# Kernel optimization log

Hardware: AMD Instinct MI355X
Metric: run time of the kernel (lower is better)

Reference implementation:

```python
import jax, jax.numpy as jnp
import numpy as np

KS = 3   # window kernel size
NH = 4   # num heads

def unfold3d(x, ks):
    # x: (B,C,D,H,W) -> (B,C,D*H*W, ks**3); matches torch unfold(2).unfold(3).unfold(4) ordering
    B, C, D, H, W = x.shape
    p = ks // 2
    xp = jnp.pad(x, ((0,0),(0,0),(p,p),(p,p),(p,p)))
    wins = [xp[:, :, i:i+D, j:j+H, k:k+W]
            for i in range(ks) for j in range(ks) for k in range(ks)]
    u = jnp.stack(wins, axis=-1)  # (B,C,D,H,W,ks^3)
    return u.reshape(B, C, D*H*W, ks**3)

def make_mask(D, H, W, ks):
    ones = jnp.ones((1, 1, D, H, W), jnp.float32)
    return unfold3d(ones, ks)[0, 0] == 0  # (N, ks^3), True = out-of-bounds (masked)

def l2norm(x, eps=1e-12):
    n = jnp.sqrt(jnp.sum(x * x, axis=-1, keepdims=True))
    return x / jnp.maximum(n, eps)

def layernorm(x, g, b, eps=1e-5):
    m = x.mean(-1, keepdims=True)
    v = x.var(-1, keepdims=True)
    return (x - m) / jnp.sqrt(v + eps) * g + b

def conv3d(x, w, b, pad):
    y = jax.lax.conv_general_dilated(x, w, (1,1,1), [(pad,pad)]*3,
        dimension_numbers=('NCDHW', 'OIDHW', 'NCDHW'))
    return y + b.reshape(1, -1, 1, 1, 1)

def bnorm(x, g, b, eps=1e-5):
    # BatchNorm3d, training-mode batch statistics (biased variance)
    m = x.mean(axis=(0,2,3,4), keepdims=True)
    v = ((x - m) ** 2).mean(axis=(0,2,3,4), keepdims=True)
    return (x - m) / jnp.sqrt(v + eps) * g.reshape(1,-1,1,1,1) + b.reshape(1,-1,1,1,1)

def lrelu(x):
    return jnp.where(x > 0, x, 0.01 * x)

def resblock(x, w1, b1, g1, be1, w2, b2, g2, be2):
    # monai UnetResBlock, in==out, stride 1 -> identity residual
    y = lrelu(bnorm(conv3d(x, w1, b1, 1), g1, be1))
    y = bnorm(conv3d(y, w2, b2, 1), g2, be2)
    return lrelu(y + x)

def epa(x, D, H, W, mask, qkvv_w, temp, temp2, rpb, qemb, op1_w, op1_b, op2_w, op2_b):
    B, N, C = x.shape
    hd = C // NH
    qkvv = (x @ qkvv_w.T).reshape(B, N, 4, NH, hd).transpose(2, 0, 3, 1, 4)  # (4,B,NH,N,hd)
    q, k, v_ca, v_sa = qkvv[0], qkvv[1], qkvv[2], qkvv[3]
    # ---- spatial (local window) attention ----
    qns = (l2norm(q) + qemb) * jax.nn.softplus(temp2)  # (B,NH,N,hd)
    k_flat = k.transpose(0, 1, 3, 2).reshape(B, C, N)
    v_flat = v_sa.transpose(0, 1, 3, 2).reshape(B, C, N)
    k_loc = unfold3d(k_flat.reshape(B, C, D, H, W), KS).reshape(B, NH, hd, N, KS**3).transpose(0, 1, 3, 2, 4)
    v_loc = unfold3d(v_flat.reshape(B, C, D, H, W), KS).reshape(B, NH, hd, N, KS**3).transpose(0, 1, 3, 2, 4)
    attn_sa = jnp.einsum('bhnd,bhndk->bhnk', qns, k_loc) + rpb[None, :, None, :]
    attn_sa = jnp.where(mask[None, None], -jnp.inf, attn_sa)
    attn_sa = jax.nn.softmax(attn_sa, axis=-1)
    # NOTE: original torch code reshapes (B,NH,N,hd) directly to (B,N,C); replicate exactly
    x_sa = jnp.einsum('bhnk,bhndk->bhnd', attn_sa, v_loc).reshape(B, N, C)
    # ---- channel (cosine) cross-attention ----
    qt = l2norm(q.transpose(0, 1, 3, 2))  # (B,NH,hd,N), normalized over N
    kt = l2norm(k.transpose(0, 1, 3, 2))
    attn_ca = jax.nn.softmax(jnp.einsum('bhdn,bhen->bhde', qt, kt) * temp, axis=-1)
    x_ca = jnp.einsum('bhde,bhen->bhdn', attn_ca, v_ca.transpose(0, 1, 3, 2)).transpose(0, 3, 1, 2).reshape(B, N, C)
    return jnp.concatenate([x_sa @ op1_w.T + op1_b, x_ca @ op2_w.T + op2_b], axis=-1)


def setup_inputs() -> dict:
    key = jax.random.key(0)
    B, C, H, W, D = 1, 64, 32, 32, 32
    hd = C // NH
    ks = iter(jax.random.split(key, 40))
    def nrm(shape, s=0.02):
        return jax.random.normal(next(ks), shape, jnp.float32) * s
    inp = {
        'x': jax.random.normal(next(ks), (B, C, H, W, D), jnp.float32),
        'ln_g': jnp.ones((C,), jnp.float32), 'ln_b': jnp.zeros((C,), jnp.float32),
        'gamma': 1e-6 * jnp.ones((C,), jnp.float32),
        'qkvv_w': nrm((4 * C, C)),
        'temp': jnp.ones((NH, 1, 1), jnp.float32), 'temp2': jnp.ones((NH, 1, 1), jnp.float32),
        'rpb': nrm((NH, KS**3), 4e-4),
        'qemb': nrm((NH, 1, hd)),
        'op1_w': nrm((C // 2, C)), 'op1_b': jnp.zeros((C // 2,), jnp.float32),
        'op2_w': nrm((C // 2, C)), 'op2_b': jnp.zeros((C // 2,), jnp.float32),
    }
    for name in ('c51', 'c52'):
        inp[name + '_w1'] = nrm((C, C, 3, 3, 3)); inp[name + '_b1'] = jnp.zeros((C,), jnp.float32)
        inp[name + '_g1'] = jnp.ones((C,), jnp.float32); inp[name + '_be1'] = jnp.zeros((C,), jnp.float32)
        inp[name + '_w2'] = nrm((C, C, 3, 3, 3)); inp[name + '_b2'] = jnp.zeros((C,), jnp.float32)
        inp[name + '_g2'] = jnp.ones((C,), jnp.float32); inp[name + '_be2'] = jnp.zeros((C,), jnp.float32)
    inp['c8_w'] = nrm((C, C, 1, 1, 1)); inp['c8_b'] = jnp.zeros((C,), jnp.float32)
    return inp


def reference(x, ln_g, ln_b, gamma, qkvv_w, temp, temp2, rpb, qemb,
              op1_w, op1_b, op2_w, op2_b,
              c51_w1, c51_b1, c51_g1, c51_be1, c51_w2, c51_b2, c51_g2, c51_be2,
              c52_w1, c52_b1, c52_g1, c52_be1, c52_w2, c52_b2, c52_g2, c52_be2,
              c8_w, c8_b):
    B, C, H, W, D = x.shape
    N = H * W * D
    xs = x.reshape(B, C, N).transpose(0, 2, 1)  # (B,N,C)
    mask = make_mask(D, H, W, KS)
    attn = xs + gamma * epa(layernorm(xs, ln_g, ln_b), D, H, W, mask,
                            qkvv_w, temp, temp2, rpb, qemb, op1_w, op1_b, op2_w, op2_b)
    skip = attn.reshape(B, H, W, D, C).transpose(0, 4, 1, 2, 3)  # (B,C,H,W,D)
    y = resblock(skip, c51_w1, c51_b1, c51_g1, c51_be1, c51_w2, c51_b2, c51_g2, c51_be2)
    y = resblock(y, c52_w1, c52_b1, c52_g1, c52_be1, c52_w2, c52_b2, c52_g2, c52_be2)
    return skip + conv3d(y, c8_w, c8_b, 0)
```

## Files before the change

kernel.cpp:

```cpp
#include <hip/hip_runtime.h>
#include <hip/hip_bf16.h>

typedef __hip_bfloat16 bf16;
typedef __attribute__((ext_vector_type(8))) short s8v;
typedef __attribute__((ext_vector_type(4))) float f4v;

#define NTOT 32768
#define PADV 39304
#define HSZ ((size_t)NTOT*16)

__device__ __forceinline__ float bflo(unsigned int u){ union{unsigned int i;float f;}v; v.i=u<<16; return v.f; }
__device__ __forceinline__ float bfhi(unsigned int u){ union{unsigned int i;float f;}v; v.i=u&0xffff0000u; return v.f; }
__device__ __forceinline__ unsigned short f2bu(float f){ bf16 h = __float2bfloat16(f); unsigned short s; __builtin_memcpy(&s,&h,2); return s; }
__device__ __forceinline__ unsigned int pk2(float a, float b){ return (unsigned int)f2bu(a) | ((unsigned int)f2bu(b)<<16); }

__device__ __forceinline__ void load8(const bf16* p, float* o){
  uint4 u = *(const uint4*)p;
  o[0]=bflo(u.x); o[1]=bfhi(u.x); o[2]=bflo(u.y); o[3]=bfhi(u.y);
  o[4]=bflo(u.z); o[5]=bfhi(u.z); o[6]=bflo(u.w); o[7]=bfhi(u.w);
}
__device__ __forceinline__ void load16(const bf16* p, float* o){
  const uint4* q = (const uint4*)p;
  uint4 u0 = q[0], u1 = q[1];
  o[0]=bflo(u0.x); o[1]=bfhi(u0.x); o[2]=bflo(u0.y); o[3]=bfhi(u0.y);
  o[4]=bflo(u0.z); o[5]=bfhi(u0.z); o[6]=bflo(u0.w); o[7]=bfhi(u0.w);
  o[8]=bflo(u1.x); o[9]=bfhi(u1.x); o[10]=bflo(u1.y); o[11]=bfhi(u1.y);
  o[12]=bflo(u1.z); o[13]=bfhi(u1.z); o[14]=bflo(u1.w); o[15]=bfhi(u1.w);
}
__device__ __forceinline__ void store16(bf16* p, const float* v){
  uint4 u0, u1;
  u0.x=pk2(v[0],v[1]); u0.y=pk2(v[2],v[3]); u0.z=pk2(v[4],v[5]); u0.w=pk2(v[6],v[7]);
  u1.x=pk2(v[8],v[9]); u1.y=pk2(v[10],v[11]); u1.z=pk2(v[12],v[13]); u1.w=pk2(v[14],v[15]);
  uint4* q=(uint4*)p; q[0]=u0; q[1]=u1;
}

__global__ __launch_bounds__(256) void k_qkvv(const float* __restrict__ x,
    const float* __restrict__ lng, const float* __restrict__ lnb,
    const float* __restrict__ w,
    bf16* __restrict__ Qh, bf16* __restrict__ Kh, bf16* __restrict__ Vsh, bf16* __restrict__ Vch)
{
  __shared__ unsigned char sm[64000];
  float* xt = (float*)sm;
  float* mean_s = (float*)(sm + 16896);
  float* rstd_s = (float*)(sm + 16896 + 256);
  float* g_s    = (float*)(sm + 16896 + 512);
  float* b_s    = (float*)(sm + 16896 + 768);
  unsigned char* A2 = sm + 17920;
  unsigned char* Wb = sm + 27136;
  unsigned char* Cout = sm;

  int t = threadIdx.x;
  int n0 = blockIdx.x * 64;
  #pragma unroll
  for (int i=0;i<4;i++){
    int idx = t + i*256; int c = idx>>4, g = idx&15;
    *(float4*)&xt[c*66 + g*4] = *(const float4*)(x + (size_t)c*NTOT + n0 + g*4);
  }
  #pragma unroll
  for (int i=0;i<8;i++){
    int idx = t + i*256; int j = idx>>3, g = idx&7;
    float4 wa = *(const float4*)(w + (size_t)j*64 + g*8);
    float4 wb = *(const float4*)(w + (size_t)j*64 + g*8 + 4);
    uint4 u; u.x=pk2(wa.x,wa.y); u.y=pk2(wa.z,wa.w); u.z=pk2(wb.x,wb.y); u.w=pk2(wb.z,wb.w);
    *(uint4*)(Wb + j*144 + g*16) = u;
  }
  if (t<64){ g_s[t]=lng[t]; b_s[t]=lnb[t]; }
  __syncthreads();
  if (t<64){
    float s=0.f, ss=0.f;
    for (int c=0;c<64;c++){ float v=xt[c*66+t]; s+=v; ss+=v*v; }
    float m = s*(1.f/64.f);
    float var = ss*(1.f/64.f) - m*m;
    mean_s[t]=m; rstd_s[t]=rsqrtf(var+1e-5f);
  }
  __syncthreads();
  {
    int p = t>>2, c0 = (t&3)*16;
    float m = mean_s[p], rs = rstd_s[p];
    unsigned short tmp[16];
    #pragma unroll
    for (int i=0;i<16;i++){
      int c = c0+i;
      tmp[i] = f2bu((xt[c*66+p]-m)*rs*g_s[c] + b_s[c]);
    }
    *(uint4*)(A2 + p*144 + c0*2)      = *(uint4*)&tmp[0];
    *(uint4*)(A2 + p*144 + c0*2 + 16) = *(uint4*)&tmp[8];
  }
  __syncthreads();
  int wv = t>>6, lane = t&63, r = lane&15, q = lane>>4;
  f4v acc[4][4];
  #pragma unroll
  for (int mt=0;mt<4;mt++)
    #pragma unroll
    for (int nt=0;nt<4;nt++){ acc[mt][nt][0]=0.f; acc[mt][nt][1]=0.f; acc[mt][nt][2]=0.f; acc[mt][nt][3]=0.f; }
  #pragma unroll
  for (int ks=0; ks<2; ++ks){
    s8v af[4], bfr[4];
    #pragma unroll
    for (int mt=0;mt<4;mt++) af[mt] = *(const s8v*)(A2 + (mt*16+r)*144 + ks*64 + q*16);
    #pragma unroll
    for (int nt=0;nt<4;nt++) bfr[nt] = *(const s8v*)(Wb + ((wv*4+nt)*16+r)*144 + ks*64 + q*16);
    #pragma unroll
    for (int mt=0;mt<4;mt++)
      #pragma unroll
      for (int nt=0;nt<4;nt++)
        acc[mt][nt] = __builtin_amdgcn_mfma_f32_16x16x32_bf16(af[mt], bfr[nt], acc[mt][nt], 0, 0, 0);
  }
  __syncthreads();
  #pragma unroll
  for (int mt=0;mt<4;mt++)
    #pragma unroll
    for (int nt=0;nt<4;nt++){
      int j = (wv*4+nt)*16 + r;
      #pragma unroll
      for (int reg=0;reg<4;reg++){
        int p = mt*16 + q*4 + reg;
        *(unsigned short*)(Cout + p*528 + j*2) = f2bu(acc[mt][nt][reg]);
      }
    }
  __syncthreads();
  bf16* bases[4] = {Qh, Kh, Vch, Vsh};
  #pragma unroll
  for (int k=0;k<4;k++){
    int chunk = t + k*256;
    int combo = chunk >> 6, pos = chunk & 63;
    int tensor = combo >> 2, h = combo & 3;
    uint4 v = *(const uint4*)(Cout + pos*528 + (tensor*64 + h*16)*2);
    *(uint4*)((unsigned char*)bases[tensor] + ((size_t)h*HSZ + (size_t)(n0+pos)*16)*2) = v;
  }
}

__global__ __launch_bounds__(256) void k_chanpart(const bf16* __restrict__ Qh, const bf16* __restrict__ Kh,
    float* __restrict__ G, float* __restrict__ NQ, float* __restrict__ NK)
{
  int h = blockIdx.y;
  int t = threadIdx.x; int d = t>>4, e = t&15;
  __shared__ float qs[128][16];
  __shared__ float ks[128][16];
  float acc=0.f, accq=0.f, acck=0.f;
  for (int stage=0; stage<2; ++stage){
    int n0 = blockIdx.x*256 + stage*128;
    __syncthreads();
    {
      int row = t & 127, which = t >> 7;
      const bf16* p = (which ? Kh : Qh) + ((size_t)h*NTOT + n0 + row)*16;
      float tmp[16]; load16(p, tmp);
      float* dst = which ? &ks[row][0] : &qs[row][0];
      #pragma unroll
      for (int i=0;i<16;i++) dst[i]=tmp[i];
    }
    __syncthreads();
    for (int i=0;i<128;i++){
      float qv = qs[i][d], kv = ks[i][e];
      acc += qv*kv;
      if (e==0) accq += qv*qv;
      if (e==1){ float kd = ks[i][d]; acck += kd*kd; }
    }
  }
  atomicAdd(&G[(h*16+d)*16+e], acc);
  if (e==0) atomicAdd(&NQ[h*16+d], accq);
  if (e==1) atomicAdd(&NK[h*16+d], acck);
}

__global__ __launch_bounds__(256) void k_spatial(const bf16* __restrict__ Qh, const bf16* __restrict__ Kh,
    const bf16* __restrict__ Vsh, const bf16* __restrict__ Vch,
    const float* __restrict__ G, const float* __restrict__ NQ, const float* __restrict__ NK,
    const float* __restrict__ temp, const float* __restrict__ temp2,
    const float* __restrict__ rpb, const float* __restrict__ qemb,
    bf16* __restrict__ xsa, bf16* __restrict__ xca)
{
  __shared__ float aca_s[1024];
  __shared__ float rpb_s[108];
  __shared__ float qemb_s[64];
  int t = threadIdx.x;
  if (t < 64){
    int hh = t>>4;
    float tp = temp[hh];
    float nq = fmaxf(sqrtf(NQ[t]), 1e-12f);
    float sv[16]; float mx=-3.0e38f;
    #pragma unroll
    for (int e=0;e<16;e++){
      float nk = fmaxf(sqrtf(NK[hh*16+e]), 1e-12f);
      sv[e] = G[t*16+e] / (nq*nk) * tp;
      mx = fmaxf(mx, sv[e]);
    }
    float sum=0.f;
    #pragma unroll
    for (int e=0;e<16;e++){ sv[e]=expf(sv[e]-mx); sum+=sv[e]; }
    float inv = 1.f/sum;
    #pragma unroll
    for (int e=0;e<16;e++) aca_s[t*16+e] = sv[e]*inv;
  }
  if (t<108) rpb_s[t]=rpb[t];
  if (t<64) qemb_s[t]=qemb[t];
  __syncthreads();
  int lane = t & 63, h = t >> 6;
  int n = blockIdx.x*64 + lane;
  int a = n>>10, b=(n>>5)&31, c=n&31;
  const bf16* Kb = Kh + (size_t)h*HSZ;
  const bf16* Vb = Vsh + (size_t)h*HSZ;
  float q[16]; load16(Qh + (size_t)h*HSZ + (size_t)n*16, q);
  float s2=0.f;
  #pragma unroll
  for (int d=0;d<16;d++) s2 += q[d]*q[d];
  float inv = 1.f/fmaxf(sqrtf(s2), 1e-12f);
  float st2 = log1pf(expf(temp2[h]));
  #pragma unroll
  for (int d=0;d<16;d++) q[d] = (q[d]*inv + qemb_s[h*16+d])*st2;
  float sc[27]; float mx = -3.0e38f;
  #pragma unroll
  for (int kk=0;kk<27;kk++){
    int da=kk/9-1, db=(kk/3)%3-1, dc=kk%3-1;
    int aa=a+da, bb=b+db, cc=c+dc;
    float s = -3.0e38f;
    if ((unsigned)aa<32u && (unsigned)bb<32u && (unsigned)cc<32u){
      int nn = n + da*1024 + db*32 + dc;
      float kv[16]; load16(Kb + (size_t)nn*16, kv);
      s = rpb_s[h*27+kk];
      #pragma unroll
      for (int d=0;d<16;d++) s += q[d]*kv[d];
    }
    sc[kk]=s; mx = fmaxf(mx, s);
  }
  float sum=0.f;
  #pragma unroll
  for (int kk=0;kk<27;kk++){ float e = expf(sc[kk]-mx); sc[kk]=e; sum+=e; }
  float invs = 1.f/sum;
  float o[16];
  #pragma unroll
  for (int d=0;d<16;d++) o[d]=0.f;
  #pragma unroll
  for (int kk=0;kk<27;kk++){
    int da=kk/9-1, db=(kk/3)%3-1, dc=kk%3-1;
    int aa=a+da, bb=b+db, cc=c+dc;
    if ((unsigned)aa<32u && (unsigned)bb<32u && (unsigned)cc<32u){
      int nn = n + da*1024 + db*32 + dc;
      float vv[16]; load16(Vb + (size_t)nn*16, vv);
      float p = sc[kk];
      #pragma unroll
      for (int d=0;d<16;d++) o[d] += p*vv[d];
    }
  }
  #pragma unroll
  for (int d=0;d<16;d++) o[d]*=invs;
  store16(xsa + ((size_t)h*NTOT + n)*16, o);
  float vca[16]; load16(Vch + (size_t)h*HSZ + (size_t)n*16, vca);
  float oc[16];
  #pragma unroll
  for (int d=0;d<16;d++){
    float s=0.f;
    #pragma unroll
    for (int e=0;e<16;e++) s += aca_s[(h*16+d)*16+e]*vca[e];
    oc[d]=s;
  }
  store16(xca + (size_t)n*64 + h*16, oc);
}

__global__ __launch_bounds__(256) void k_epilogue(const float* __restrict__ x,
    const bf16* __restrict__ xsa, const bf16* __restrict__ xca,
    const float* __restrict__ op1w, const float* __restrict__ op1b,
    const float* __restrict__ op2w, const float* __restrict__ op2b,
    const float* __restrict__ gamma, float* __restrict__ skip)
{
  __shared__ float xs_s[64][68];
  __shared__ float xc_s[64][68];
  int t = threadIdx.x;
  int n0 = blockIdx.x * 64;
  #pragma unroll
  for (int it=0; it<2; ++it){
    int idx = t + it*256;
    int p = idx >> 3, cg = idx & 7;
    float a8[8], c8[8];
    load8(xsa + (size_t)(n0+p)*64 + cg*8, a8);
    load8(xca + (size_t)(n0+p)*64 + cg*8, c8);
    #pragma unroll
    for (int i=0;i<8;i++){ xs_s[p][cg*8+i]=a8[i]; xc_s[p][cg*8+i]=c8[i]; }
  }
  int co = t & 63, pg = t >> 6;
  const float* wrow = (co < 32) ? (op1w + (size_t)co*64) : (op2w + (size_t)(co-32)*64);
  float wreg[64];
  #pragma unroll
  for (int i=0;i<16;i++) *(float4*)&wreg[i*4] = *(const float4*)(wrow + i*4);
  float bv = (co<32) ? op1b[co] : op2b[co-32];
  float gv = gamma[co];
  __syncthreads();
  const float* xt = (co<32) ? &xs_s[0][0] : &xc_s[0][0];
  float out16[16];
  #pragma unroll
  for (int i=0;i<16;i++){
    int p = pg*16 + i;
    const float* xr = xt + p*68;
    float s = bv;
    #pragma unroll
    for (int k4=0;k4<16;k4++){
      float4 xv = *(const float4*)(xr + k4*4);
      s += wreg[k4*4]*xv.x + wreg[k4*4+1]*xv.y + wreg[k4*4+2]*xv.z + wreg[k4*4+3]*xv.w;
    }
    out16[i] = s;
  }
  size_t base = (size_t)co*NTOT + n0 + pg*16;
  #pragma unroll
  for (int i4=0;i4<4;i4++){
    float4 xv = *(const float4*)(x + base + i4*4);
    float4 ov;
    ov.x = xv.x + gv*out16[i4*4];
    ov.y = xv.y + gv*out16[i4*4+1];
    ov.z = xv.z + gv*out16[i4*4+2];
    ov.w = xv.w + gv*out16[i4*4+3];
    *(float4*)(skip + base + i4*4) = ov;
  }
}

__global__ void k_wprep(const float* __restrict__ wA, const float* __restrict__ wB_,
    const float* __restrict__ wC, const float* __restrict__ wD,
    const float* __restrict__ w8, bf16* __restrict__ WB, float* __restrict__ w8t)
{
  int idx = blockIdx.x*256 + threadIdx.x;
  if (idx < 458752){
    int j = idx & 7;
    int rr = (idx>>3) & 15;
    int q = (idx>>7) & 3;
    int nt = (idx>>9) & 3;
    int rest = idx >> 11;
    int tp = rest % 14;
    int rest2 = rest / 14;
    int cc = rest2 & 3;
    int conv = rest2 >> 2;
    int co = nt*16 + rr;
    int tap = 2*tp + (q>>1);
    int ci = cc*16 + (q&1)*8 + j;
    const float* src = conv==0?wA:conv==1?wB_:conv==2?wC:wD;
    float v = (tap < 27) ? src[((size_t)co*64 + ci)*27 + tap] : 0.f;
    WB[idx] = __float2bfloat16(v);
  }
  if (idx < 4096){ int ci = idx>>6, co = idx&63; w8t[ci*64+co] = w8[(size_t)co*64+ci]; }
}

__global__ __launch_bounds__(256) void k_padt0(const float* __restrict__ src, bf16* __restrict__ xpt)
{
  __shared__ bf16 tile[32][68];
  int t = threadIdx.x;
  int n0 = blockIdx.x * 32;
  int nl = t & 31, cig = t >> 5;
  int n = n0 + nl;
  #pragma unroll
  for (int i=0;i<8;i++){
    int ci = cig*8 + i;
    tile[nl][ci] = __float2bfloat16(src[(size_t)ci*NTOT + n]);
  }
  __syncthreads();
  int a = n0 >> 10, b = (n0 >> 5) & 31;
  size_t rowbase = ((size_t)((a+1)*34 + (b+1))*34 + 1)*64;
  #pragma unroll
  for (int k2=0;k2<2;k2++){
    int j = t + k2*256;
    int nn = j >> 4, grp = j & 15;
    uint2 val = *(const uint2*)&tile[nn][grp*4];
    *(uint2*)((unsigned char*)xpt + (rowbase + (size_t)nn*64 + grp*4)*2) = val;
  }
}

__global__ __launch_bounds__(256) void k_padtbn(const bf16* __restrict__ src,
    const float* __restrict__ stats, const float* __restrict__ g, const float* __restrict__ be,
    const float* __restrict__ skipin, bf16* __restrict__ xpt)
{
  __shared__ bf16 tile[32][68];
  int t = threadIdx.x;
  int n0 = blockIdx.x * 32;
  int nl = t & 31, cig = t >> 5;
  int n = n0 + nl;
  #pragma unroll
  for (int i=0;i<8;i++){
    int ci = cig*8 + i;
    float S = stats[ci*2], SS = stats[ci*2+1];
    float m = S*(1.f/NTOT);
    float rs = rsqrtf(SS*(1.f/NTOT) - m*m + 1e-5f);
    float v = __bfloat162float(src[(size_t)ci*NTOT + n]);
    v = (v-m)*rs*g[ci] + be[ci];
    if (skipin) v += skipin[(size_t)ci*NTOT + n];
    v = v>0.f ? v : 0.01f*v;
    tile[nl][ci] = __float2bfloat16(v);
  }
  __syncthreads();
  int a = n0 >> 10, b = (n0 >> 5) & 31;
  size_t rowbase = ((size_t)((a+1)*34 + (b+1))*34 + 1)*64;
  #pragma unroll
  for (int k2=0;k2<2;k2++){
    int j = t + k2*256;
    int nn = j >> 4, grp = j & 15;
    uint2 val = *(const uint2*)&tile[nn][grp*4];
    *(uint2*)((unsigned char*)xpt + (rowbase + (size_t)nn*64 + grp*4)*2) = val;
  }
}

__global__ __launch_bounds__(256, 2) void k_conv3m(const bf16* __restrict__ xpt,
    const bf16* __restrict__ WB, const float* __restrict__ bias,
    bf16* __restrict__ Yb, float* __restrict__ BNpart)
{
  __shared__ float smf[17408];
  unsigned char* smb = (unsigned char*)smf;
  int t = threadIdx.x;
  int w = t >> 6, lane = t & 63;
  int r = lane & 15, q = lane >> 4;
  int qe = q & 1, qh = q >> 1;
  int xcd = blockIdx.x & 7, loc = blockIdx.x >> 3;
  int a = xcd*4 + (loc>>4), b0 = (loc&15)*2;

  {
    uint4 tmp[13];
    #pragma unroll
    for (int k=0;k<13;k++){
      int idx = t + k*256;
      if (idx < 3264){
        int pos = idx >> 3, h = idx & 7;
        int par = pos/136, rem = pos - par*136;
        int pbr = rem/34, pc = rem - pbr*34;
        size_t gb = (((size_t)(a+par)*34 + (b0+pbr))*34 + pc)*128 + h*16;
        tmp[k] = *(const uint4*)((const unsigned char*)xpt + gb);
      }
    }
    #pragma unroll
    for (int k=0;k<13;k++){
      int idx = t + k*256;
      if (idx < 3264){
        int pos = idx >> 3, h = idx & 7;
        *(uint4*)(smb + pos*144 + h*16) = tmp[k];
      }
    }
  }

  int toff[14];
  #pragma unroll
  for (int tp=0;tp<14;++tp){
    int tap = 2*tp + qh;
    int da = tap/9, rem = tap - da*9, db = rem/3, dc = rem - db*3;
    toff[tp] = (tap<27) ? (((da*4+db)*34 + dc)*144) : 0;
  }
  int F[4];
  #pragma unroll
  for (int mt=0;mt<4;mt++) F[mt] = (((mt>>1)*34 + (mt&1)*16 + r)*144) + w*32 + qe*16;
  const unsigned char* wbp = (const unsigned char*)WB + (size_t)w*57344 + lane*16;

  f4v acc[4][4];
  #pragma unroll
  for (int mt=0;mt<4;mt++)
    #pragma unroll
    for (int nt=0;nt<4;nt++){ acc[mt][nt][0]=0.f; acc[mt][nt][1]=0.f; acc[mt][nt][2]=0.f; acc[mt][nt][3]=0.f; }

  __syncthreads();

  s8v aC[4], bC[4], bN[4];
  #pragma unroll
  for (int mt=0;mt<4;mt++) aC[mt] = *(const s8v*)(smb + F[mt] + toff[0]);
  #pragma unroll
  for (int nt=0;nt<4;nt++){ bC[nt] = *(const s8v*)(wbp + nt*1024); bN[nt] = *(const s8v*)(wbp + 4096 + nt*1024); }

  #pragma unroll
  for (int tp=0; tp<14; ++tp){
    s8v aN[4], bN2[4];
    if (tp < 12){
      #pragma unroll
      for (int nt=0;nt<4;nt++) bN2[nt] = *(const s8v*)(wbp + (tp+2)*4096 + nt*1024);
    }
    if (tp < 13){
      #pragma unroll
      for (int mt=0;mt<4;mt++) aN[mt] = *(const s8v*)(smb + F[mt] + toff[tp+1]);
    }
    #pragma unroll
    for (int mt=0;mt<4;mt++)
      #pragma unroll
      for (int nt=0;nt<4;nt++)
        acc[mt][nt] = __builtin_amdgcn_mfma_f32_16x16x32_bf16(aC[mt], bC[nt], acc[mt][nt], 0, 0, 0);
    #pragma unroll
    for (int nt=0;nt<4;nt++) bC[nt] = bN[nt];
    if (tp < 12){
      #pragma unroll
      for (int nt=0;nt<4;nt++) bN[nt] = bN2[nt];
    }
    if (tp < 13){
      #pragma unroll
      for (int mt=0;mt<4;mt++) aC[mt] = aN[mt];
    }
  }

  __syncthreads();
  #pragma unroll
  for (int mt=0;mt<4;mt++)
    #pragma unroll
    for (int nt=0;nt<4;nt++)
      *(float4*)&smf[w*4352 + (nt*16+r)*68 + mt*16 + q*4] = *(float4*)&acc[mt][nt];
  __syncthreads();

  {
    int co = t >> 2, pg = t & 3;
    float bv = bias[co];
    float vals[16];
    #pragma unroll
    for (int i4=0;i4<4;i4++){
      int p = pg*16 + i4*4;
      float4 s0 = *(const float4*)&smf[0*4352 + co*68 + p];
      float4 s1 = *(const float4*)&smf[1*4352 + co*68 + p];
      float4 s2 = *(const float4*)&smf[2*4352 + co*68 + p];
      float4 s3 = *(const float4*)&smf[3*4352 + co*68 + p];
      vals[i4*4+0] = s0.x+s1.x+s2.x+s3.x+bv;
      vals[i4*4+1] = s0.y+s1.y+s2.y+s3.y+bv;
      vals[i4*4+2] = s0.z+s1.z+s2.z+s3.z+bv;
      vals[i4*4+3] = s0.w+s1.w+s2.w+s3.w+bv;
    }
    float s=0.f, ss=0.f;
    #pragma unroll
    for (int i=0;i<16;i++){ s+=vals[i]; ss+=vals[i]*vals[i]; }
    s += __shfl_xor(s,1); ss += __shfl_xor(ss,1);
    s += __shfl_xor(s,2); ss += __shfl_xor(ss,2);
    if (pg==0){
      BNpart[(size_t)blockIdx.x*128 + co*2]     = s;
      BNpart[(size_t)blockIdx.x*128 + co*2 + 1] = ss;
    }
    uint4 u0, u1;
    u0.x=pk2(vals[0],vals[1]); u0.y=pk2(vals[2],vals[3]); u0.z=pk2(vals[4],vals[5]); u0.w=pk2(vals[6],vals[7]);
    u1.x=pk2(vals[8],vals[9]); u1.y=pk2(vals[10],vals[11]); u1.z=pk2(vals[12],vals[13]); u1.w=pk2(vals[14],vals[15]);
    size_t nb = (size_t)co*NTOT + (size_t)a*1024 + b0*32 + pg*16;
    uint4* dst = (uint4*)((unsigned char*)Yb + nb*2);
    dst[0] = u0; dst[1] = u1;
  }
}

__global__ __launch_bounds__(1024) void k_bnred(const float* __restrict__ BNpart, float* __restrict__ BNout)
{
  __shared__ float red[8][128];
  int t = threadIdx.x;
  int col = t & 127, grp = t >> 7;
  float acc = 0.f;
  #pragma unroll 8
  for (int r = grp*64; r < grp*64 + 64; ++r) acc += BNpart[r*128 + col];
  red[grp][col] = acc;
  __syncthreads();
  if (grp == 0){
    float s = 0.f;
    #pragma unroll
    for (int g=0; g<8; g++) s += red[g][col];
    BNout[col] = s;
  }
}

__global__ __launch_bounds__(256) void k_conv1f(const bf16* __restrict__ Y2b,
    const float* __restrict__ BNst, const float* __restrict__ g, const float* __restrict__ be,
    const bf16* __restrict__ xptR, const float* __restrict__ w8t, const float* __restrict__ b8,
    const float* __restrict__ skip, float* __restrict__ out)
{
  __shared__ unsigned short xptt[64][72];
  __shared__ float R2[64][68];
  __shared__ float wt[4096];
  __shared__ float bs[64];
  int t = threadIdx.x;
  int n0 = blockIdx.x * 64;
  int a = n0 >> 10, b0 = (n0 >> 5) & 31;
  {
    int p = t >> 2, seg = t & 3;
    int pb = b0 + (p >> 5) + 1, pc = (p & 31) + 1;
    size_t rowb = (((size_t)(a+1)*34 + pb)*34 + pc)*128;
    uint4 v0 = *(const uint4*)((const unsigned char*)xptR + rowb + seg*32);
    uint4 v1 = *(const uint4*)((const unsigned char*)xptR + rowb + seg*32 + 16);
    *(uint4*)((unsigned char*)&xptt[p][seg*16]) = v0;
    *(uint4*)((unsigned char*)&xptt[p][seg*16 + 8]) = v1;
  }
  #pragma unroll
  for (int k=0;k<4;k++){
    int idx = t + k*256;
    *(float4*)&wt[idx*4] = *(const float4*)(w8t + idx*4);
  }
  if (t < 64) bs[t] = b8[t];
  __syncthreads();
  {
    int ci = t >> 2, pg = t & 3;
    float S = BNst[ci*2], SS = BNst[ci*2+1];
    float m = S*(1.f/NTOT);
    float rs = rsqrtf(SS*(1.f/NTOT) - m*m + 1e-5f);
    float gv = g[ci], bev = be[ci];
    float y16[16];
    load16(Y2b + (size_t)ci*NTOT + n0 + pg*16, y16);
    #pragma unroll
    for (int i=0;i<16;i++){
      int nl = pg*16 + i;
      unsigned short us = xptt[nl][ci];
      union{unsigned int ui; float f;} cv; cv.ui = ((unsigned int)us)<<16;
      float v = (y16[i]-m)*rs*gv + bev + cv.f;
      R2[ci][nl] = v>0.f ? v : 0.01f*v;
    }
  }
  __syncthreads();
  int lane = t & 63, cg = t >> 6;
  float acc[16];
  #pragma unroll
  for (int j=0;j<16;j++) acc[j]=0.f;
  for (int ci=0; ci<64; ci++){
    float rv = R2[ci][lane];
    const float* wr = &wt[ci*64 + cg*16];
    float4 wa = *(const float4*)(wr);
    float4 wb = *(const float4*)(wr+4);
    float4 wc = *(const float4*)(wr+8);
    float4 wd = *(const float4*)(wr+12);
    acc[0]+=rv*wa.x; acc[1]+=rv*wa.y; acc[2]+=rv*wa.z; acc[3]+=rv*wa.w;
    acc[4]+=rv*wb.x; acc[5]+=rv*wb.y; acc[6]+=rv*wb.z; acc[7]+=rv*wb.w;
    acc[8]+=rv*wc.x; acc[9]+=rv*wc.y; acc[10]+=rv*wc.z; acc[11]+=rv*wc.w;
    acc[12]+=rv*wd.x; acc[13]+=rv*wd.y; acc[14]+=rv*wd.z; acc[15]+=rv*wd.w;
  }
  #pragma unroll
  for (int j=0;j<16;j++){
    int co = cg*16+j;
    out[(size_t)co*NTOT + n0 + lane] = acc[j] + bs[co] + skip[(size_t)co*NTOT + n0 + lane];
  }
}

extern "C" void kernel_launch(void* const* d_in, const int* in_sizes, int n_in,
                              void* d_out, int out_size, void* d_ws, size_t ws_size,
                              hipStream_t stream) {
  (void)in_sizes; (void)n_in; (void)out_size; (void)ws_size;
  const float* x      = (const float*)d_in[0];
  const float* ln_g   = (const float*)d_in[1];
  const float* ln_b   = (const float*)d_in[2];
  const float* gamma  = (const float*)d_in[3];
  const float* qkvv_w = (const float*)d_in[4];
  const float* temp   = (const float*)d_in[5];
  const float* temp2  = (const float*)d_in[6];
  const float* rpb    = (const float*)d_in[7];
  const float* qemb   = (const float*)d_in[8];
  const float* op1w   = (const float*)d_in[9];
  const float* op1b   = (const float*)d_in[10];
  const float* op2w   = (const float*)d_in[11];
  const float* op2b   = (const float*)d_in[12];
  const float* c51_w1 = (const float*)d_in[13];
  const float* c51_b1 = (const float*)d_in[14];
  const float* c51_g1 = (const float*)d_in[15];
  const float* c51_be1= (const float*)d_in[16];
  const float* c51_w2 = (const float*)d_in[17];
  const float* c51_b2 = (const float*)d_in[18];
  const float* c51_g2 = (const float*)d_in[19];
  const float* c51_be2= (const float*)d_in[20];
  const float* c52_w1 = (const float*)d_in[21];
  const float* c52_b1 = (const float*)d_in[22];
  const float* c52_g1 = (const float*)d_in[23];
  const float* c52_be1= (const float*)d_in[24];
  const float* c52_w2 = (const float*)d_in[25];
  const float* c52_b2 = (const float*)d_in[26];
  const float* c52_g2 = (const float*)d_in[27];
  const float* c52_be2= (const float*)d_in[28];
  const float* c8_w   = (const float*)d_in[29];
  const float* c8_b   = (const float*)d_in[30];

  unsigned char* ws = (unsigned char*)d_ws;
  const size_t MB = 1u<<20;
  bf16*  Qh   = (bf16*)(ws + 0);
  bf16*  Kh   = (bf16*)(ws + 4*MB);
  bf16*  Vsh  = (bf16*)(ws + 8*MB);
  bf16*  Vch  = (bf16*)(ws + 12*MB);
  bf16*  xpt  = (bf16*)(ws + 0);
  bf16*  xpt2 = (bf16*)(ws + 5030912);
  bf16*  xsa  = (bf16*)(ws + 16*MB);
  bf16*  xca  = (bf16*)(ws + 20*MB);
  float* skip = (float*)(ws + 24*MB);
  float* stat = (float*)(ws + 32*MB);
  float* G    = stat + 0;
  float* NQ   = stat + 1024;
  float* NK   = stat + 1088;
  float* BN1  = stat + 1152;
  float* BN2  = stat + 1312;
  float* BN3  = stat + 1472;
  float* BN4  = stat + 1632;
  bf16*  WB   = (bf16*)(ws + 32*MB + 65536);
  float* w8t  = (float*)(ws + 32*MB + 65536 + 1835008);
  float* BNpart = (float*)(ws + 34*MB);
  bf16*  Yb   = (bf16*)(ws + 35*MB);
  bf16*  Y2b  = (bf16*)(ws + 39*MB);

  hipMemsetAsync(stat, 0, 1152*sizeof(float), stream);
  k_wprep<<<1792,256,0,stream>>>(c51_w1, c51_w2, c52_w1, c52_w2, c8_w, WB, w8t);
  k_qkvv<<<512,256,0,stream>>>(x, ln_g, ln_b, qkvv_w, Qh, Kh, Vsh, Vch);
  k_chanpart<<<dim3(128,4),256,0,stream>>>(Qh, Kh, G, NQ, NK);
  k_spatial<<<512,256,0,stream>>>(Qh, Kh, Vsh, Vch, G, NQ, NK, temp, temp2, rpb, qemb, xsa, xca);
  k_epilogue<<<512,256,0,stream>>>(x, xsa, xca, op1w, op1b, op2w, op2b, gamma, skip);
  hipMemsetAsync(ws, 0, 2*5030912, stream);
  k_padt0 <<<1024,256,0,stream>>>(skip, xpt);
  k_conv3m<<<512,256,0,stream>>>(xpt, WB + 0*114688, c51_b1, Yb, BNpart);
  k_bnred<<<1,1024,0,stream>>>(BNpart, BN1);
  k_padtbn<<<1024,256,0,stream>>>(Yb, BN1, c51_g1, c51_be1, nullptr, xpt);
  k_conv3m<<<512,256,0,stream>>>(xpt, WB + 1*114688, c51_b2, Y2b, BNpart);
  k_bnred<<<1,1024,0,stream>>>(BNpart, BN2);
  k_padtbn<<<1024,256,0,stream>>>(Y2b, BN2, c51_g2, c51_be2, skip, xpt);
  k_conv3m<<<512,256,0,stream>>>(xpt, WB + 2*114688, c52_b1, Yb, BNpart);
  k_bnred<<<1,1024,0,stream>>>(BNpart, BN3);
  k_padtbn<<<1024,256,0,stream>>>(Yb, BN3, c52_g1, c52_be1, nullptr, xpt2);
  k_conv3m<<<512,256,0,stream>>>(xpt2, WB + 3*114688, c52_b2, Y2b, BNpart);
  k_bnred<<<1,1024,0,stream>>>(BNpart, BN4);
  k_conv1f<<<512,256,0,stream>>>(Y2b, BN4, c52_g2, c52_be2, xpt, w8t, c8_b, skip, (float*)d_out);
}
```

Baseline: 317.0 us.

## Fuse BN/LReLU/pad prologue into conv kernels and switch to channels-last layouts

Removes the separate padding/BN-apply kernels and the padded-buffer memset. Each 3x3x3 conv now loads its input halo directly from an unpadded channels-last tensor, applying the previous BatchNorm, residual add and LeakyReLU on the fly with zero-fill at the borders. The epilogue and conv outputs are transposed through shared memory so they are written channels-last. The final 1x1 conv recomputes the first resblock's output from Y2 and the BN2 stats, so no padded copy is needed. This cuts several launches and a full-tensor write/read per stage, at the cost of extra shared-memory transposes and redundant BN math inside the conv halo loads.

```diff
diff --git a/kernel.cpp b/kernel.cpp
--- a/kernel.cpp
+++ b/kernel.cpp
@@ -6,7 +6,6 @@
 typedef __attribute__((ext_vector_type(4))) float f4v;
 
 #define NTOT 32768
-#define PADV 39304
 #define HSZ ((size_t)NTOT*16)
 
 __device__ __forceinline__ float bflo(unsigned int u){ union{unsigned int i;float f;}v; v.i=u<<16; return v.f; }
@@ -260,10 +259,11 @@
     const bf16* __restrict__ xsa, const bf16* __restrict__ xca,
     const float* __restrict__ op1w, const float* __restrict__ op1b,
     const float* __restrict__ op2w, const float* __restrict__ op2b,
-    const float* __restrict__ gamma, float* __restrict__ skip)
+    const float* __restrict__ gamma, float* __restrict__ skipf)
 {
   __shared__ float xs_s[64][68];
   __shared__ float xc_s[64][68];
+  __shared__ float trans[64][68];
   int t = threadIdx.x;
   int n0 = blockIdx.x * 64;
   #pragma unroll
@@ -302,12 +302,20 @@
   #pragma unroll
   for (int i4=0;i4<4;i4++){
     float4 xv = *(const float4*)(x + base + i4*4);
-    float4 ov;
-    ov.x = xv.x + gv*out16[i4*4];
-    ov.y = xv.y + gv*out16[i4*4+1];
-    ov.z = xv.z + gv*out16[i4*4+2];
-    ov.w = xv.w + gv*out16[i4*4+3];
-    *(float4*)(skip + base + i4*4) = ov;
+    out16[i4*4]   = xv.x + gv*out16[i4*4];
+    out16[i4*4+1] = xv.y + gv*out16[i4*4+1];
+    out16[i4*4+2] = xv.z + gv*out16[i4*4+2];
+    out16[i4*4+3] = xv.w + gv*out16[i4*4+3];
+  }
+  #pragma unroll
+  for (int i=0;i<16;i++) trans[pg*16+i][co] = out16[i];
+  __syncthreads();
+  {
+    int pos = t >> 2, grp = t & 3;
+    float* dst = skipf + (size_t)(n0+pos)*64 + grp*16;
+    #pragma unroll
+    for (int i4=0;i4<4;i4++)
+      *(float4*)(dst + i4*4) = *(const float4*)&trans[pos][grp*16 + i4*4];
   }
 }
 
@@ -336,66 +344,12 @@
   if (idx < 4096){ int ci = idx>>6, co = idx&63; w8t[ci*64+co] = w8[(size_t)co*64+ci]; }
 }
 
-__global__ __launch_bounds__(256) void k_padt0(const float* __restrict__ src, bf16* __restrict__ xpt)
-{
-  __shared__ bf16 tile[32][68];
-  int t = threadIdx.x;
-  int n0 = blockIdx.x * 32;
-  int nl = t & 31, cig = t >> 5;
-  int n = n0 + nl;
-  #pragma unroll
-  for (int i=0;i<8;i++){
-    int ci = cig*8 + i;
-    tile[nl][ci] = __float2bfloat16(src[(size_t)ci*NTOT + n]);
-  }
-  __syncthreads();
-  int a = n0 >> 10, b = (n0 >> 5) & 31;
-  size_t rowbase = ((size_t)((a+1)*34 + (b+1))*34 + 1)*64;
-  #pragma unroll
-  for (int k2=0;k2<2;k2++){
-    int j = t + k2*256;
-    int nn = j >> 4, grp = j & 15;
-    uint2 val = *(const uint2*)&tile[nn][grp*4];
-    *(uint2*)((unsigned char*)xpt + (rowbase + (size_t)nn*64 + grp*4)*2) = val;
-  }
-}
-
-__global__ __launch_bounds__(256) void k_padtbn(const bf16* __restrict__ src,
+template<int MODE>
+__global__ __launch_bounds__(256, 2) void k_conv3x(const void* __restrict__ src,
     const float* __restrict__ stats, const float* __restrict__ g, const float* __restrict__ be,
-    const float* __restrict__ skipin, bf16* __restrict__ xpt)
-{
-  __shared__ bf16 tile[32][68];
-  int t = threadIdx.x;
-  int n0 = blockIdx.x * 32;
-  int nl = t & 31, cig = t >> 5;
-  int n = n0 + nl;
-  #pragma unroll
-  for (int i=0;i<8;i++){
-    int ci = cig*8 + i;
-    float S = stats[ci*2], SS = stats[ci*2+1];
-    float m = S*(1.f/NTOT);
-    float rs = rsqrtf(SS*(1.f/NTOT) - m*m + 1e-5f);
-    float v = __bfloat162float(src[(size_t)ci*NTOT + n]);
-    v = (v-m)*rs*g[ci] + be[ci];
-    if (skipin) v += skipin[(size_t)ci*NTOT + n];
-    v = v>0.f ? v : 0.01f*v;
-    tile[nl][ci] = __float2bfloat16(v);
-  }
-  __syncthreads();
-  int a = n0 >> 10, b = (n0 >> 5) & 31;
-  size_t rowbase = ((size_t)((a+1)*34 + (b+1))*34 + 1)*64;
-  #pragma unroll
-  for (int k2=0;k2<2;k2++){
-    int j = t + k2*256;
-    int nn = j >> 4, grp = j & 15;
-    uint2 val = *(const uint2*)&tile[nn][grp*4];
-    *(uint2*)((unsigned char*)xpt + (rowbase + (size_t)nn*64 + grp*4)*2) = val;
-  }
-}
-
-__global__ __launch_bounds__(256, 2) void k_conv3m(const bf16* __restrict__ xpt,
+    const float* __restrict__ resid,
     const bf16* __restrict__ WB, const float* __restrict__ bias,
-    bf16* __restrict__ Yb, float* __restrict__ BNpart)
+    bf16* __restrict__ Yout, float* __restrict__ BNpart)
 {
   __shared__ float smf[17408];
   unsigned char* smb = (unsigned char*)smf;
@@ -403,28 +357,113 @@
   int w = t >> 6, lane = t & 63;
   int r = lane & 15, q = lane >> 4;
   int qe = q & 1, qh = q >> 1;
-  int xcd = blockIdx.x & 7, loc = blockIdx.x >> 3;
-  int a = xcd*4 + (loc>>4), b0 = (loc&15)*2;
-
-  {
-    uint4 tmp[13];
-    #pragma unroll
-    for (int k=0;k<13;k++){
-      int idx = t + k*256;
-      if (idx < 3264){
-        int pos = idx >> 3, h = idx & 7;
-        int par = pos/136, rem = pos - par*136;
-        int pbr = rem/34, pc = rem - pbr*34;
-        size_t gb = (((size_t)(a+par)*34 + (b0+pbr))*34 + pc)*128 + h*16;
-        tmp[k] = *(const uint4*)((const unsigned char*)xpt + gb);
+  int a = blockIdx.x >> 4, b0 = (blockIdx.x & 15) * 2;
+  int hh = t & 7;
+
+  float m8[8], rs8[8], be8[8];
+  if (MODE != 0){
+    #pragma unroll
+    for (int i=0;i<8;i++){
+      int ci = hh*8 + i;
+      float S = stats[ci*2], SS = stats[ci*2+1];
+      float m = S*(1.f/NTOT);
+      m8[i] = m;
+      rs8[i] = rsqrtf(SS*(1.f/NTOT) - m*m + 1e-5f) * g[ci];
+      be8[i] = be[ci];
+    }
+  }
+
+  if (MODE == 0){
+    #pragma unroll
+    for (int c0=0;c0<2;++c0){
+      int kb = c0*7, kn = (c0==0)?7:6;
+      float4 f0[7], f1[7]; int fl[7];
+      #pragma unroll
+      for (int k=0;k<7;k++){
+        fl[k]=0;
+        if (k<kn){
+          int idx = t + (kb+k)*256;
+          if (idx < 3264){
+            int pos = idx>>3;
+            int par=pos/136, rem=pos-par*136, pbr=rem/34, pc=rem-pbr*34;
+            int pa=a+par, pb=b0+pbr;
+            fl[k]=1;
+            if (pa>=1&&pa<=32&&pb>=1&&pb<=32&&pc>=1&&pc<=32){
+              int nsrc=(pa-1)*1024+(pb-1)*32+(pc-1);
+              const float* p = (const float*)src + (size_t)nsrc*64 + hh*8;
+              f0[k]=*(const float4*)p; f1[k]=*(const float4*)(p+4);
+              fl[k]=2;
+            }
+          }
+        }
       }
-    }
-    #pragma unroll
-    for (int k=0;k<13;k++){
-      int idx = t + k*256;
-      if (idx < 3264){
-        int pos = idx >> 3, h = idx & 7;
-        *(uint4*)(smb + pos*144 + h*16) = tmp[k];
+      #pragma unroll
+      for (int k=0;k<7;k++){
+        if (k<kn && fl[k]){
+          int pos = (t + (kb+k)*256)>>3;
+          uint4 o={0,0,0,0};
+          if (fl[k]==2){
+            o.x=pk2(f0[k].x,f0[k].y); o.y=pk2(f0[k].z,f0[k].w);
+            o.z=pk2(f1[k].x,f1[k].y); o.w=pk2(f1[k].z,f1[k].w);
+          }
+          *(uint4*)(smb + pos*144 + hh*16) = o;
+        }
+      }
+    }
+  } else {
+    const int CS = (MODE==2)?5:13;
+    const int NC = (MODE==2)?3:1;
+    #pragma unroll
+    for (int c0=0;c0<NC;++c0){
+      int kb = c0*CS;
+      int kn = (MODE==2) ? ((c0==2)?3:5) : 13;
+      uint4 u[CS]; float4 r0[CS], r1[CS]; int fl[CS];
+      #pragma unroll
+      for (int k=0;k<CS;k++){
+        fl[k]=0;
+        if (k<kn){
+          int idx = t + (kb+k)*256;
+          if (idx < 3264){
+            int pos = idx>>3;
+            int par=pos/136, rem=pos-par*136, pbr=rem/34, pc=rem-pbr*34;
+            int pa=a+par, pb=b0+pbr;
+            fl[k]=1;
+            if (pa>=1&&pa<=32&&pb>=1&&pb<=32&&pc>=1&&pc<=32){
+              int nsrc=(pa-1)*1024+(pb-1)*32+(pc-1);
+              u[k] = *(const uint4*)((const unsigned char*)src + ((size_t)nsrc*64 + hh*8)*2);
+              if (MODE==2){
+                const float* rp = resid + (size_t)nsrc*64 + hh*8;
+                r0[k]=*(const float4*)rp; r1[k]=*(const float4*)(rp+4);
+              }
+              fl[k]=2;
+            }
+          }
+        }
+      }
+      #pragma unroll
+      for (int k=0;k<CS;k++){
+        if (k<kn && fl[k]){
+          int pos = (t + (kb+k)*256)>>3;
+          uint4 o={0,0,0,0};
+          if (fl[k]==2){
+            float v[8];
+            v[0]=bflo(u[k].x); v[1]=bfhi(u[k].x); v[2]=bflo(u[k].y); v[3]=bfhi(u[k].y);
+            v[4]=bflo(u[k].z); v[5]=bfhi(u[k].z); v[6]=bflo(u[k].w); v[7]=bfhi(u[k].w);
+            float rv[8];
+            if (MODE==2){
+              rv[0]=r0[k].x; rv[1]=r0[k].y; rv[2]=r0[k].z; rv[3]=r0[k].w;
+              rv[4]=r1[k].x; rv[5]=r1[k].y; rv[6]=r1[k].z; rv[7]=r1[k].w;
+            }
+            #pragma unroll
+            for (int i=0;i<8;i++){
+              float y = (v[i]-m8[i])*rs8[i] + be8[i];
+              if (MODE==2) y += rv[i];
+              v[i] = y>0.f ? y : 0.01f*y;
+            }
+            o.x=pk2(v[0],v[1]); o.y=pk2(v[2],v[3]); o.z=pk2(v[4],v[5]); o.w=pk2(v[6],v[7]);
+          }
+          *(uint4*)(smb + pos*144 + hh*16) = o;
+        }
       }
     }
   }
@@ -491,10 +530,10 @@
       *(float4*)&smf[w*4352 + (nt*16+r)*68 + mt*16 + q*4] = *(float4*)&acc[mt][nt];
   __syncthreads();
 
+  float vals[16];
   {
     int co = t >> 2, pg = t & 3;
     float bv = bias[co];
-    float vals[16];
     #pragma unroll
     for (int i4=0;i4<4;i4++){
       int p = pg*16 + i4*4;
@@ -516,11 +555,24 @@
       BNpart[(size_t)blockIdx.x*128 + co*2]     = s;
       BNpart[(size_t)blockIdx.x*128 + co*2 + 1] = ss;
     }
+  }
+  __syncthreads();
+  {
+    int co = t >> 2, pg = t & 3;
+    #pragma unroll
+    for (int i=0;i<16;i++) smf[(pg*16+i)*68 + co] = vals[i];
+  }
+  __syncthreads();
+  {
+    int pos = t >> 2, grp = t & 3;
+    float v16[16];
+    #pragma unroll
+    for (int i4=0;i4<4;i4++) *(float4*)&v16[i4*4] = *(const float4*)&smf[pos*68 + grp*16 + i4*4];
     uint4 u0, u1;
-    u0.x=pk2(vals[0],vals[1]); u0.y=pk2(vals[2],vals[3]); u0.z=pk2(vals[4],vals[5]); u0.w=pk2(vals[6],vals[7]);
-    u1.x=pk2(vals[8],vals[9]); u1.y=pk2(vals[10],vals[11]); u1.z=pk2(vals[12],vals[13]); u1.w=pk2(vals[14],vals[15]);
-    size_t nb = (size_t)co*NTOT + (size_t)a*1024 + b0*32 + pg*16;
-    uint4* dst = (uint4*)((unsigned char*)Yb + nb*2);
+    u0.x=pk2(v16[0],v16[1]); u0.y=pk2(v16[2],v16[3]); u0.z=pk2(v16[4],v16[5]); u0.w=pk2(v16[6],v16[7]);
+    u1.x=pk2(v16[8],v16[9]); u1.y=pk2(v16[10],v16[11]); u1.z=pk2(v16[12],v16[13]); u1.w=pk2(v16[14],v16[15]);
+    int nb = a*1024 + (b0 + (pos>>5))*32 + (pos&31);
+    uint4* dst = (uint4*)((unsigned char*)Yout + ((size_t)nb*64 + grp*16)*2);
     dst[0] = u0; dst[1] = u1;
   }
 }
@@ -543,49 +595,48 @@
   }
 }
 
-__global__ __launch_bounds__(256) void k_conv1f(const bf16* __restrict__ Y2b,
-    const float* __restrict__ BNst, const float* __restrict__ g, const float* __restrict__ be,
-    const bf16* __restrict__ xptR, const float* __restrict__ w8t, const float* __restrict__ b8,
-    const float* __restrict__ skip, float* __restrict__ out)
+__global__ __launch_bounds__(256) void k_conv1f(const bf16* __restrict__ Y4,
+    const float* __restrict__ BN4, const float* __restrict__ g4, const float* __restrict__ be4,
+    const bf16* __restrict__ Y2, const float* __restrict__ BN2,
+    const float* __restrict__ g2, const float* __restrict__ be2,
+    const float* __restrict__ skipf, const float* __restrict__ w8t, const float* __restrict__ b8,
+    float* __restrict__ out)
 {
-  __shared__ unsigned short xptt[64][72];
   __shared__ float R2[64][68];
+  __shared__ float skT[64][68];
   __shared__ float wt[4096];
   __shared__ float bs[64];
   int t = threadIdx.x;
   int n0 = blockIdx.x * 64;
-  int a = n0 >> 10, b0 = (n0 >> 5) & 31;
-  {
-    int p = t >> 2, seg = t & 3;
-    int pb = b0 + (p >> 5) + 1, pc = (p & 31) + 1;
-    size_t rowb = (((size_t)(a+1)*34 + pb)*34 + pc)*128;
-    uint4 v0 = *(const uint4*)((const unsigned char*)xptR + rowb + seg*32);
-    uint4 v1 = *(const uint4*)((const unsigned char*)xptR + rowb + seg*32 + 16);
-    *(uint4*)((unsigned char*)&xptt[p][seg*16]) = v0;
-    *(uint4*)((unsigned char*)&xptt[p][seg*16 + 8]) = v1;
-  }
   #pragma unroll
   for (int k=0;k<4;k++){
     int idx = t + k*256;
     *(float4*)&wt[idx*4] = *(const float4*)(w8t + idx*4);
   }
   if (t < 64) bs[t] = b8[t];
-  __syncthreads();
   {
-    int ci = t >> 2, pg = t & 3;
-    float S = BNst[ci*2], SS = BNst[ci*2+1];
-    float m = S*(1.f/NTOT);
-    float rs = rsqrtf(SS*(1.f/NTOT) - m*m + 1e-5f);
-    float gv = g[ci], bev = be[ci];
-    float y16[16];
-    load16(Y2b + (size_t)ci*NTOT + n0 + pg*16, y16);
+    int pos = t >> 2, grp = t & 3;
+    int n = n0 + pos;
+    float y2[16], y4[16], sk[16];
+    load16(Y2 + (size_t)n*64 + grp*16, y2);
+    load16(Y4 + (size_t)n*64 + grp*16, y4);
+    #pragma unroll
+    for (int i4=0;i4<4;i4++) *(float4*)&sk[i4*4] = *(const float4*)(skipf + (size_t)n*64 + grp*16 + i4*4);
     #pragma unroll
     for (int i=0;i<16;i++){
-      int nl = pg*16 + i;
-      unsigned short us = xptt[nl][ci];
-      union{unsigned int ui; float f;} cv; cv.ui = ((unsigned int)us)<<16;
-      float v = (y16[i]-m)*rs*gv + bev + cv.f;
-      R2[ci][nl] = v>0.f ? v : 0.01f*v;
+      int ci = grp*16+i;
+      float S2=BN2[ci*2], SS2=BN2[ci*2+1];
+      float m2=S2*(1.f/NTOT);
+      float r2v=rsqrtf(SS2*(1.f/NTOT)-m2*m2+1e-5f);
+      float R = (y2[i]-m2)*r2v*g2[ci]+be2[ci] + sk[i];
+      R = R>0.f ? R : 0.01f*R;
+      float S4=BN4[ci*2], SS4=BN4[ci*2+1];
+      float m4=S4*(1.f/NTOT);
+      float r4v=rsqrtf(SS4*(1.f/NTOT)-m4*m4+1e-5f);
+      float vy = (y4[i]-m4)*r4v*g4[ci]+be4[ci] + R;
+      vy = vy>0.f ? vy : 0.01f*vy;
+      R2[ci][pos] = vy;
+      skT[ci][pos] = sk[i];
     }
   }
   __syncthreads();
@@ -608,7 +659,7 @@
   #pragma unroll
   for (int j=0;j<16;j++){
     int co = cg*16+j;
-    out[(size_t)co*NTOT + n0 + lane] = acc[j] + bs[co] + skip[(size_t)co*NTOT + n0 + lane];
+    out[(size_t)co*NTOT + n0 + lane] = acc[j] + bs[co] + skT[co][lane];
   }
 }
 
@@ -654,11 +705,9 @@
   bf16*  Kh   = (bf16*)(ws + 4*MB);
   bf16*  Vsh  = (bf16*)(ws + 8*MB);
   bf16*  Vch  = (bf16*)(ws + 12*MB);
-  bf16*  xpt  = (bf16*)(ws + 0);
-  bf16*  xpt2 = (bf16*)(ws + 5030912);
   bf16*  xsa  = (bf16*)(ws + 16*MB);
   bf16*  xca  = (bf16*)(ws + 20*MB);
-  float* skip = (float*)(ws + 24*MB);
+  float* skipf= (float*)(ws + 24*MB);
   float* stat = (float*)(ws + 32*MB);
   float* G    = stat + 0;
   float* NQ   = stat + 1024;
@@ -667,30 +716,27 @@
   float* BN2  = stat + 1312;
   float* BN3  = stat + 1472;
   float* BN4  = stat + 1632;
-  bf16*  WB   = (bf16*)(ws + 32*MB + 65536);
-  float* w8t  = (float*)(ws + 32*MB + 65536 + 1835008);
-  float* BNpart = (float*)(ws + 34*MB);
-  bf16*  Yb   = (bf16*)(ws + 35*MB);
-  bf16*  Y2b  = (bf16*)(ws + 39*MB);
+  bf16*  WB   = (bf16*)(ws + 33*MB);
+  float* w8t  = (float*)(ws + 33*MB + 1048576);
+  float* BNpart = (float*)(ws + 35*MB);
+  bf16*  Y1   = (bf16*)(ws + 36*MB);
+  bf16*  Y2   = (bf16*)(ws + 40*MB);
+  bf16*  Y3   = (bf16*)(ws + 44*MB);
+  bf16*  Y4   = (bf16*)(ws + 48*MB);
 
   hipMemsetAsync(stat, 0, 1152*sizeof(float), stream);
   k_wprep<<<1792,256,0,stream>>>(c51_w1, c51_w2, c52_w1, c52_w2, c8_w, WB, w8t);
   k_qkvv<<<512,256,0,stream>>>(x, ln_g, ln_b, qkvv_w, Qh, Kh, Vsh, Vch);
   k_chanpart<<<dim3(128,4),256,0,stream>>>(Qh, Kh, G, NQ, NK);
   k_spatial<<<512,256,0,stream>>>(Qh, Kh, Vsh, Vch, G, NQ, NK, temp, temp2, rpb, qemb, xsa, xca);
-  k_epilogue<<<512,256,0,stream>>>(x, xsa, xca, op1w, op1b, op2w, op2b, gamma, skip);
-  hipMemsetAsync(ws, 0, 2*5030912, stream);
-  k_padt0 <<<1024,256,0,stream>>>(skip, xpt);
-  k_conv3m<<<512,256,0,stream>>>(xpt, WB + 0*114688, c51_b1, Yb, BNpart);
+  k_epilogue<<<512,256,0,stream>>>(x, xsa, xca, op1w, op1b, op2w, op2b, gamma, skipf);
+  k_conv3x<0><<<512,256,0,stream>>>(skipf, nullptr, nullptr, nullptr, nullptr, WB + 0*114688, c51_b1, Y1, BNpart);
   k_bnred<<<1,1024,0,stream>>>(BNpart, BN1);
-  k_padtbn<<<1024,256,0,stream>>>(Yb, BN1, c51_g1, c51_be1, nullptr, xpt);
-  k_conv3m<<<512,256,0,stream>>>(xpt, WB + 1*114688, c51_b2, Y2b, BNpart);
+  k_conv3x<1><<<512,256,0,stream>>>(Y1, BN1, c51_g1, c51_be1, nullptr, WB + 1*114688, c51_b2, Y2, BNpart);
   k_bnred<<<1,1024,0,stream>>>(BNpart, BN2);
-  k_padtbn<<<1024,256,0,stream>>>(Y2b, BN2, c51_g2, c51_be2, skip, xpt);
-  k_conv3m<<<512,256,0,stream>>>(xpt, WB + 2*114688, c52_b1, Yb, BNpart);
+  k_conv3x<2><<<512,256,0,stream>>>(Y2, BN2, c51_g2, c51_be2, skipf, WB + 2*114688, c52_b1, Y3, BNpart);
   k_bnred<<<1,1024,0,stream>>>(BNpart, BN3);
-  k_padtbn<<<1024,256,0,stream>>>(Yb, BN3, c52_g1, c52_be1, nullptr, xpt2);
-  k_conv3m<<<512,256,0,stream>>>(xpt2, WB + 3*114688, c52_b2, Y2b, BNpart);
+  k_conv3x<1><<<512,256,0,stream>>>(Y3, BN3, c52_g1, c52_be1, nullptr, WB + 3*114688, c52_b2, Y4, BNpart);
   k_bnred<<<1,1024,0,stream>>>(BNpart, BN4);
-  k_conv1f<<<512,256,0,stream>>>(Y2b, BN4, c52_g2, c52_be2, xpt, w8t, c8_b, skip, (float*)d_out);
-}
+  k_conv1f<<<512,256,0,stream>>>(Y4, BN4, c52_g2, c52_be2, Y2, BN2, c51_g2, c51_be2, skipf, w8t, c8_b, (float*)d_out);
+}
```

Result: faster. 288.4 us (-9.0%).
